# Performance work log

Hardware: AMD Instinct MI355X
Metric: run time of the kernel (lower is better)

Reference implementation:

```python
import jax, jax.numpy as jnp
import numpy as np

S, D, H1, H2, H3 = 4, 384, 160, 128, 96  # species, aev_length, hidden dims
B, A = 2048, 64  # conformations, atoms
CELU_ALPHA = 0.1


def setup_inputs() -> dict:
    key = jax.random.key(0)
    ks = jax.random.split(key, 10)
    scale = 0.1
    return {
        "species": jax.random.randint(ks[0], (B, A), 0, S),
        "aev": jax.random.normal(ks[1], (B, A, D), dtype=jnp.float32),
        "W1": jax.random.normal(ks[2], (S, D, H1), dtype=jnp.float32) * scale,
        "b1": jax.random.normal(ks[3], (S, H1), dtype=jnp.float32) * scale,
        "W2": jax.random.normal(ks[4], (S, H1, H2), dtype=jnp.float32) * scale,
        "b2": jax.random.normal(ks[5], (S, H2), dtype=jnp.float32) * scale,
        "W3": jax.random.normal(ks[6], (S, H2, H3), dtype=jnp.float32) * scale,
        "b3": jax.random.normal(ks[7], (S, H3), dtype=jnp.float32) * scale,
        "W4": jax.random.normal(ks[8], (S, H3, 1), dtype=jnp.float32) * scale,
        "b4": jax.random.normal(ks[9], (S, 1), dtype=jnp.float32) * scale,
    }


def _celu(x):
    return jax.nn.celu(x, alpha=CELU_ALPHA)


def reference(species, aev, W1, b1, W2, b2, W3, b3, W4, b4):
    # species: [B, A] int; aev: [B, A, D]
    b, a, d = aev.shape
    x = aev.reshape(b * a, d)  # flatten(0, 1)
    # Run every species-expert MLP on all atoms (dense, jit-friendly), then
    # gather the row matching each atom's species. Same math as the masked
    # index_select/scatter loop in the original (padding_fill=0, reducer=sum).
    h = _celu(jnp.einsum('nd,sdh->snh', x, W1) + b1[:, None, :])   # [S, N, H1]
    h = _celu(jnp.einsum('snh,sho->sno', h, W2) + b2[:, None, :])  # [S, N, H2]
    h = _celu(jnp.einsum('snh,sho->sno', h, W3) + b3[:, None, :])  # [S, N, H3]
    y = (jnp.einsum('snh,sho->sno', h, W4) + b4[:, None, :])[..., 0]  # [S, N]
    sp_flat = species.reshape(1, b * a)
    per_atom = jnp.take_along_axis(y, sp_flat, axis=0)[0]  # [N]
    per_atom = per_atom.reshape(b, a)
    energies = per_atom.sum(axis=1)  # reducer=torch.sum over dim=1
    return species, energies
```

## Files before the change

kernel.cpp:

```cpp
#include <hip/hip_runtime.h>
#include <hip/hip_bf16.h>


#define NSP   4
#define DIM   384
#define NH1   160
#define NH2   128
#define NH3   96
#define DIMP  392
#define NH1P  168
#define NH2P  136
#define NH3P  104
#define NATOM (2048 * 64)
#define NCONF 2048

typedef __attribute__((ext_vector_type(8))) short short8;
typedef __attribute__((ext_vector_type(4))) float f32x4;

__device__ __forceinline__ unsigned short f2bf(float f) {
  union { float f; unsigned u; } v; v.f = f;
  unsigned r = v.u + 0x7fffu + ((v.u >> 16) & 1u);
  return (unsigned short)(r >> 16);
}
__device__ __forceinline__ float bf2f(unsigned short h) {
  union { unsigned u; float f; } v; v.u = ((unsigned)h) << 16;
  return v.f;
}


__global__ void k_count(const int* __restrict__ sp, int* __restrict__ hdr,
                        float* __restrict__ out_species) {
  const int i = blockIdx.x * 256 + threadIdx.x;
  const int s = sp[i];
  out_species[i] = (float)s;
  __shared__ int cnt[NSP];
  if (threadIdx.x < NSP) cnt[threadIdx.x] = 0;
  __syncthreads();
  const int lane = threadIdx.x & 63;
#pragma unroll
  for (int sv = 0; sv < NSP; ++sv) {
    unsigned long long m = __ballot(s == sv);
    if (lane == 0) atomicAdd(&cnt[sv], __popcll(m));
  }
  __syncthreads();
  if (threadIdx.x < NSP) atomicAdd(&hdr[threadIdx.x], cnt[threadIdx.x]);
}

__global__ void k_scan(int* hdr) {
  if (threadIdx.x == 0 && blockIdx.x == 0) {
    int ro = 0, po = 0;
    for (int s = 0; s < NSP; ++s) {
      hdr[4 + s]  = ro;
      hdr[9 + s]  = po;
      hdr[14 + s] = ro;
      int cs = hdr[s];
      ro += cs;
      po += (cs + 63) & ~63;
    }
    hdr[8]  = ro;
    hdr[13] = po;
  }
}

__global__ void k_scatter(const int* __restrict__ sp, int* __restrict__ hdr,
                          int* __restrict__ sorted) {
  const int i = blockIdx.x * 256 + threadIdx.x;
  const int s = sp[i];
  const int lane = threadIdx.x & 63, wave = threadIdx.x >> 6;
  __shared__ int wcnt[4][NSP];
  __shared__ int wbase[4][NSP];
  const unsigned long long below = (1ull << lane) - 1ull;
  int myrank = 0;
#pragma unroll
  for (int sv = 0; sv < NSP; ++sv) {
    unsigned long long m = __ballot(s == sv);
    if (sv == s) myrank = __popcll(m & below);
    if (lane == 0) wcnt[wave][sv] = __popcll(m);
  }
  __syncthreads();
  if (threadIdx.x < NSP) {
    const int sv = threadIdx.x;
    const int tot = wcnt[0][sv] + wcnt[1][sv] + wcnt[2][sv] + wcnt[3][sv];
    int off = atomicAdd(&hdr[14 + sv], tot);
#pragma unroll
    for (int w = 0; w < 4; ++w) { wbase[w][sv] = off; off += wcnt[w][sv]; }
  }
  __syncthreads();
  sorted[wbase[wave][s] + myrank] = i;
}

__global__ void k_wcvt(const float* __restrict__ src, unsigned short* __restrict__ dst,
                       int K, int N, int total) {
  int i = blockIdx.x * 256 + threadIdx.x;
  if (i < total) {
    int kn = K * N;
    int s = i / kn, r = i - s * kn;
    int n = r / K, k = r - n * K;
    dst[i] = f2bf(src[s * kn + k * N + n]);
  }
}


template <int K, int KP, int NOUT, int NOUTP, bool DOCELU>
__device__ __forceinline__ void layer(const unsigned short* __restrict__ sIn,
                                      const unsigned short* __restrict__ Wt,
                                      const float* __restrict__ bias,
                                      unsigned short* __restrict__ sOut,
                                      int wave, int lane) {
  constexpr int NF = NOUT / 16;
  constexpr int NOWN = (NF + 3) / 4;
  const int c = lane & 15, q = lane >> 4;
  const int kb = q * 8;

  f32x4 acc[4][NOWN];
#pragma unroll
  for (int m = 0; m < 4; ++m)
#pragma unroll
    for (int i = 0; i < NOWN; ++i) acc[m][i] = (f32x4){0.f, 0.f, 0.f, 0.f};

  for (int k0 = 0; k0 < K; k0 += 32) {
    short8 a[4];
#pragma unroll
    for (int m = 0; m < 4; ++m)
      a[m] = *(const short8*)(sIn + (m * 16 + c) * KP + k0 + kb);
#pragma unroll
    for (int i = 0; i < NOWN; ++i) {
      int f = wave + 4 * i;
      if (f < NF) {
        short8 b = *(const short8*)(Wt + (f * 16 + c) * K + k0 + kb);
#pragma unroll
        for (int m = 0; m < 4; ++m)
          acc[m][i] = __builtin_amdgcn_mfma_f32_16x16x32_bf16(a[m], b, acc[m][i], 0, 0, 0);
      }
    }
  }

#pragma unroll
  for (int i = 0; i < NOWN; ++i) {
    int f = wave + 4 * i;
    if (f < NF) {
      int col = f * 16 + c;
      float bv = bias[col];
#pragma unroll
      for (int m = 0; m < 4; ++m) {
#pragma unroll
        for (int j = 0; j < 4; ++j) {
          float v = acc[m][i][j] + bv;
          if (DOCELU) v = v > 0.f ? v : 0.1f * (__expf(10.f * v) - 1.f);
          sOut[(m * 16 + q * 4 + j) * NOUTP + col] = f2bf(v);
        }
      }
    }
  }
}

#define LDSA (64 * DIMP * 2)
#define LDSH (64 * NH1P * 2)

__global__ __launch_bounds__(256) void k_mlp(
    const int* __restrict__ hdr, const int* __restrict__ sorted,
    const float* __restrict__ aev,
    const unsigned short* __restrict__ Wt1, const unsigned short* __restrict__ Wt2,
    const unsigned short* __restrict__ Wt3,
    const float* __restrict__ b1, const float* __restrict__ b2,
    const float* __restrict__ b3,
    const float* __restrict__ W4, const float* __restrict__ b4,
    float* __restrict__ energy) {
  __shared__ __align__(16) unsigned char smem[LDSA + LDSH];
  unsigned short* sA = (unsigned short*)smem;
  unsigned short* sH = (unsigned short*)(smem + LDSA);

  const int tid = threadIdx.x, wave = tid >> 6, lane = tid & 63;
  const int t64 = blockIdx.x << 6;
  if (t64 >= hdr[13]) return;
  const int s = (t64 >= hdr[10]) + (t64 >= hdr[11]) + (t64 >= hdr[12]);
  const int seg0 = t64 - hdr[9 + s];
  const int base = hdr[4 + s] + seg0;
  const int cnt = hdr[s];

  for (int rr = 0; rr < 16; ++rr) {
    const int row = (wave << 4) + rr;
    const bool valid = (seg0 + row) < cnt;
    const int atom = valid ? sorted[base + row] : 0;
    const float4* src = (const float4*)(aev + (size_t)atom * DIM);
#pragma unroll
    for (int jj = 0; jj < 2; ++jj) {
      const int idx = lane + (jj << 6);
      if (idx < 96) {
        float4 v = valid ? src[idx] : make_float4(0.f, 0.f, 0.f, 0.f);
        uint2 w;
        w.x = (unsigned)f2bf(v.x) | ((unsigned)f2bf(v.y) << 16);
        w.y = (unsigned)f2bf(v.z) | ((unsigned)f2bf(v.w) << 16);
        *(uint2*)(sA + row * DIMP + idx * 4) = w;
      }
    }
  }
  __syncthreads();

  layer<DIM, DIMP, NH1, NH1P, true>(sA, Wt1 + s * NH1 * DIM, b1 + s * NH1, sH, wave, lane);
  __syncthreads();
  layer<NH1, NH1P, NH2, NH2P, true>(sH, Wt2 + s * NH2 * NH1, b2 + s * NH2, sA, wave, lane);
  __syncthreads();
  layer<NH2, NH2P, NH3, NH3P, true>(sA, Wt3 + s * NH3 * NH2, b3 + s * NH3, sH, wave, lane);
  __syncthreads();

  {
    const int row = tid >> 2, part = tid & 3;
    if (seg0 + row < cnt) {
      const float* w4 = W4 + s * NH3 + part * 24;
      const unsigned short* hrow = sH + row * NH3P + part * 24;
      float acc = 0.f;
#pragma unroll
      for (int u = 0; u < 3; ++u) {
        short8 h = *(const short8*)(hrow + u * 8);
#pragma unroll
        for (int e = 0; e < 8; ++e)
          acc += bf2f((unsigned short)h[e]) * w4[u * 8 + e];
      }
      acc += __shfl_xor(acc, 1);
      acc += __shfl_xor(acc, 2);
      if (part == 0) {
        const int atom = sorted[base + row];
        atomicAdd(&energy[atom >> 6], acc + b4[s]);
      }
    }
  }
}


extern "C" void kernel_launch(void* const* d_in, const int* in_sizes, int n_in,
                              void* d_out, int out_size, void* d_ws, size_t ws_size,
                              hipStream_t stream) {
  const int* species = (const int*)d_in[0];
  const float* aev = (const float*)d_in[1];
  const float* W1 = (const float*)d_in[2];
  const float* b1 = (const float*)d_in[3];
  const float* W2 = (const float*)d_in[4];
  const float* b2 = (const float*)d_in[5];
  const float* W3 = (const float*)d_in[6];
  const float* b3 = (const float*)d_in[7];
  const float* W4 = (const float*)d_in[8];
  const float* b4 = (const float*)d_in[9];

  int* hdr = (int*)d_ws;
  int* sorted = (int*)((char*)d_ws + 128);
  unsigned short* Wt1 = (unsigned short*)((char*)d_ws + 128 + (size_t)NATOM * 4);
  unsigned short* Wt2 = Wt1 + NSP * NH1 * DIM;
  unsigned short* Wt3 = Wt2 + NSP * NH2 * NH1;

  float* out_species = (float*)d_out;
  float* energy = (float*)d_out + NATOM;

  hipMemsetAsync(d_ws, 0, 128, stream);
  hipMemsetAsync(energy, 0, NCONF * sizeof(float), stream);

  k_count<<<NATOM / 256, 256, 0, stream>>>(species, hdr, out_species);
  k_scan<<<1, 64, 0, stream>>>(hdr);
  k_scatter<<<NATOM / 256, 256, 0, stream>>>(species, hdr, sorted);
  k_wcvt<<<(NSP * NH1 * DIM + 255) / 256, 256, 0, stream>>>(W1, Wt1, DIM, NH1, NSP * NH1 * DIM);
  k_wcvt<<<(NSP * NH2 * NH1 + 255) / 256, 256, 0, stream>>>(W2, Wt2, NH1, NH2, NSP * NH2 * NH1);
  k_wcvt<<<(NSP * NH3 * NH2 + 255) / 256, 256, 0, stream>>>(W3, Wt3, NH2, NH3, NSP * NH3 * NH2);

  k_mlp<<<2052, 256, 0, stream>>>(hdr, sorted, aev, Wt1, Wt2, Wt3,
                                  b1, b2, b3, W4, b4, energy);
}
```

Before: 504.0 us.

## Give each wave its own 16-row tile, read AEV directly into MFMA operands

```diff
diff --git a/kernel.cpp b/kernel.cpp
--- a/kernel.cpp
+++ b/kernel.cpp
@@ -7,13 +7,17 @@
 #define NH1   160
 #define NH2   128
 #define NH3   96
-#define DIMP  392
 #define NH1P  168
 #define NH2P  136
 #define NH3P  104
 #define NATOM (2048 * 64)
 #define NCONF 2048
 
+#define XBYTES (16 * NH1P * 2)
+#define YBYTES (16 * NH2P * 2)
+#define WAVE_LDS (XBYTES + YBYTES)
+#define BLOCK_LDS (4 * WAVE_LDS)
+
 typedef __attribute__((ext_vector_type(8))) short short8;
 typedef __attribute__((ext_vector_type(4))) float f32x4;
 
@@ -25,6 +29,17 @@
 __device__ __forceinline__ float bf2f(unsigned short h) {
   union { unsigned u; float f; } v; v.u = ((unsigned)h) << 16;
   return v.f;
+}
+__device__ __forceinline__ short8 cvt8(float4 x, float4 y) {
+  union { short8 v; __hip_bfloat162 h[4]; } u;
+  u.h[0] = __float22bfloat162_rn(make_float2(x.x, x.y));
+  u.h[1] = __float22bfloat162_rn(make_float2(x.z, x.w));
+  u.h[2] = __float22bfloat162_rn(make_float2(y.x, y.y));
+  u.h[3] = __float22bfloat162_rn(make_float2(y.z, y.w));
+  return u.v;
+}
+__device__ __forceinline__ float celu01(float v) {
+  return v > 0.f ? v : 0.1f * (__expf(10.f * v) - 1.f);
 }
 
 
@@ -89,75 +104,60 @@
   sorted[wbase[wave][s] + myrank] = i;
 }
 
-__global__ void k_wcvt(const float* __restrict__ src, unsigned short* __restrict__ dst,
-                       int K, int N, int total) {
+#define N1TOT (NSP * NH1 * DIM)
+#define N2TOT (NSP * NH2 * NH1)
+#define N3TOT (NSP * NH3 * NH2)
+#define NWTOT (N1TOT + N2TOT + N3TOT)
+
+__device__ __forceinline__ void wcvt1(const float* src, unsigned short* dst,
+                                      int i, int K, int N) {
+  int kn = K * N;
+  int s = i / kn, r = i - s * kn;
+  int n = r / K, k = r - n * K;
+  dst[i] = f2bf(src[s * kn + k * N + n]);
+}
+
+__global__ void k_wcvt_all(const float* __restrict__ W1, const float* __restrict__ W2,
+                           const float* __restrict__ W3,
+                           unsigned short* __restrict__ Wt1, unsigned short* __restrict__ Wt2,
+                           unsigned short* __restrict__ Wt3) {
   int i = blockIdx.x * 256 + threadIdx.x;
-  if (i < total) {
-    int kn = K * N;
-    int s = i / kn, r = i - s * kn;
-    int n = r / K, k = r - n * K;
-    dst[i] = f2bf(src[s * kn + k * N + n]);
-  }
-}
-
-
-template <int K, int KP, int NOUT, int NOUTP, bool DOCELU>
-__device__ __forceinline__ void layer(const unsigned short* __restrict__ sIn,
-                                      const unsigned short* __restrict__ Wt,
-                                      const float* __restrict__ bias,
-                                      unsigned short* __restrict__ sOut,
-                                      int wave, int lane) {
+  if (i < N1TOT) wcvt1(W1, Wt1, i, DIM, NH1);
+  else if (i < N1TOT + N2TOT) wcvt1(W2, Wt2, i - N1TOT, NH1, NH2);
+  else if (i < NWTOT) wcvt1(W3, Wt3, i - N1TOT - N2TOT, NH2, NH3);
+}
+
+
+template <int K, int KP, int NOUT, int NOUTP>
+__device__ __forceinline__ void layerL(const unsigned short* __restrict__ sIn,
+                                       const unsigned short* __restrict__ Wt,
+                                       const float* __restrict__ bias,
+                                       unsigned short* __restrict__ sOut,
+                                       int c, int q) {
   constexpr int NF = NOUT / 16;
-  constexpr int NOWN = (NF + 3) / 4;
-  const int c = lane & 15, q = lane >> 4;
-  const int kb = q * 8;
-
-  f32x4 acc[4][NOWN];
-#pragma unroll
-  for (int m = 0; m < 4; ++m)
-#pragma unroll
-    for (int i = 0; i < NOWN; ++i) acc[m][i] = (f32x4){0.f, 0.f, 0.f, 0.f};
-
+  f32x4 acc[NF];
+#pragma unroll
+  for (int f = 0; f < NF; ++f) acc[f] = (f32x4){0.f, 0.f, 0.f, 0.f};
+
+#pragma unroll 2
   for (int k0 = 0; k0 < K; k0 += 32) {
-    short8 a[4];
-#pragma unroll
-    for (int m = 0; m < 4; ++m)
-      a[m] = *(const short8*)(sIn + (m * 16 + c) * KP + k0 + kb);
-#pragma unroll
-    for (int i = 0; i < NOWN; ++i) {
-      int f = wave + 4 * i;
-      if (f < NF) {
-        short8 b = *(const short8*)(Wt + (f * 16 + c) * K + k0 + kb);
-#pragma unroll
-        for (int m = 0; m < 4; ++m)
-          acc[m][i] = __builtin_amdgcn_mfma_f32_16x16x32_bf16(a[m], b, acc[m][i], 0, 0, 0);
-      }
-    }
-  }
-
-#pragma unroll
-  for (int i = 0; i < NOWN; ++i) {
-    int f = wave + 4 * i;
-    if (f < NF) {
-      int col = f * 16 + c;
-      float bv = bias[col];
-#pragma unroll
-      for (int m = 0; m < 4; ++m) {
-#pragma unroll
-        for (int j = 0; j < 4; ++j) {
-          float v = acc[m][i][j] + bv;
-          if (DOCELU) v = v > 0.f ? v : 0.1f * (__expf(10.f * v) - 1.f);
-          sOut[(m * 16 + q * 4 + j) * NOUTP + col] = f2bf(v);
-        }
-      }
-    }
-  }
-}
-
-#define LDSA (64 * DIMP * 2)
-#define LDSH (64 * NH1P * 2)
-
-__global__ __launch_bounds__(256) void k_mlp(
+    short8 a = *(const short8*)(sIn + c * KP + k0 + q * 8);
+#pragma unroll
+    for (int f = 0; f < NF; ++f) {
+      short8 b = *(const short8*)(Wt + (f * 16 + c) * K + k0 + q * 8);
+      acc[f] = __builtin_amdgcn_mfma_f32_16x16x32_bf16(a, b, acc[f], 0, 0, 0);
+    }
+  }
+#pragma unroll
+  for (int f = 0; f < NF; ++f) {
+    float bv = bias[f * 16 + c];
+#pragma unroll
+    for (int j = 0; j < 4; ++j)
+      sOut[(4 * q + j) * NOUTP + f * 16 + c] = f2bf(celu01(acc[f][j] + bv));
+  }
+}
+
+__global__ __launch_bounds__(256, 4) void k_mlp(
     const int* __restrict__ hdr, const int* __restrict__ sorted,
     const float* __restrict__ aev,
     const unsigned short* __restrict__ Wt1, const unsigned short* __restrict__ Wt2,
@@ -166,64 +166,66 @@
     const float* __restrict__ b3,
     const float* __restrict__ W4, const float* __restrict__ b4,
     float* __restrict__ energy) {
-  __shared__ __align__(16) unsigned char smem[LDSA + LDSH];
-  unsigned short* sA = (unsigned short*)smem;
-  unsigned short* sH = (unsigned short*)(smem + LDSA);
-
+  __shared__ __align__(16) unsigned char smem[BLOCK_LDS];
   const int tid = threadIdx.x, wave = tid >> 6, lane = tid & 63;
+  const int c = lane & 15, q = lane >> 4;
+  unsigned short* hX = (unsigned short*)(smem + wave * WAVE_LDS);
+  unsigned short* hY = (unsigned short*)(smem + wave * WAVE_LDS + XBYTES);
+
   const int t64 = blockIdx.x << 6;
   if (t64 >= hdr[13]) return;
   const int s = (t64 >= hdr[10]) + (t64 >= hdr[11]) + (t64 >= hdr[12]);
-  const int seg0 = t64 - hdr[9 + s];
-  const int base = hdr[4 + s] + seg0;
-  const int cnt = hdr[s];
-
-  for (int rr = 0; rr < 16; ++rr) {
-    const int row = (wave << 4) + rr;
-    const bool valid = (seg0 + row) < cnt;
-    const int atom = valid ? sorted[base + row] : 0;
-    const float4* src = (const float4*)(aev + (size_t)atom * DIM);
-#pragma unroll
-    for (int jj = 0; jj < 2; ++jj) {
-      const int idx = lane + (jj << 6);
-      if (idx < 96) {
-        float4 v = valid ? src[idx] : make_float4(0.f, 0.f, 0.f, 0.f);
-        uint2 w;
-        w.x = (unsigned)f2bf(v.x) | ((unsigned)f2bf(v.y) << 16);
-        w.y = (unsigned)f2bf(v.z) | ((unsigned)f2bf(v.w) << 16);
-        *(uint2*)(sA + row * DIMP + idx * 4) = w;
+  const int seg0 = t64 - hdr[9 + s] + wave * 16;
+  const int cnt  = hdr[s];
+  const bool valid = (seg0 + c) < cnt;
+  const int sidx = valid ? (hdr[4 + s] + seg0 + c) : hdr[4 + s];
+  const int atom = sorted[sidx];
+  const float* __restrict__ arow = aev + (size_t)atom * DIM;
+
+  {
+    const unsigned short* __restrict__ Wt = Wt1 + s * NH1 * DIM;
+    f32x4 acc[10];
+#pragma unroll
+    for (int f = 0; f < 10; ++f) acc[f] = (f32x4){0.f, 0.f, 0.f, 0.f};
+#pragma unroll 2
+    for (int k0 = 0; k0 < DIM; k0 += 32) {
+      float4 fa = *(const float4*)(arow + k0 + q * 8);
+      float4 fb = *(const float4*)(arow + k0 + q * 8 + 4);
+      short8 a = cvt8(fa, fb);
+#pragma unroll
+      for (int f = 0; f < 10; ++f) {
+        short8 b = *(const short8*)(Wt + (f * 16 + c) * DIM + k0 + q * 8);
+        acc[f] = __builtin_amdgcn_mfma_f32_16x16x32_bf16(a, b, acc[f], 0, 0, 0);
       }
     }
-  }
-  __syncthreads();
-
-  layer<DIM, DIMP, NH1, NH1P, true>(sA, Wt1 + s * NH1 * DIM, b1 + s * NH1, sH, wave, lane);
-  __syncthreads();
-  layer<NH1, NH1P, NH2, NH2P, true>(sH, Wt2 + s * NH2 * NH1, b2 + s * NH2, sA, wave, lane);
-  __syncthreads();
-  layer<NH2, NH2P, NH3, NH3P, true>(sA, Wt3 + s * NH3 * NH2, b3 + s * NH3, sH, wave, lane);
-  __syncthreads();
+    const float* bias = b1 + s * NH1;
+#pragma unroll
+    for (int f = 0; f < 10; ++f) {
+      float bv = bias[f * 16 + c];
+#pragma unroll
+      for (int j = 0; j < 4; ++j)
+        hX[(4 * q + j) * NH1P + f * 16 + c] = f2bf(celu01(acc[f][j] + bv));
+    }
+  }
+
+  layerL<NH1, NH1P, NH2, NH2P>(hX, Wt2 + s * NH2 * NH1, b2 + s * NH2, hY, c, q);
+  layerL<NH2, NH2P, NH3, NH3P>(hY, Wt3 + s * NH3 * NH2, b3 + s * NH3, hX, c, q);
 
   {
-    const int row = tid >> 2, part = tid & 3;
-    if (seg0 + row < cnt) {
-      const float* w4 = W4 + s * NH3 + part * 24;
-      const unsigned short* hrow = sH + row * NH3P + part * 24;
-      float acc = 0.f;
-#pragma unroll
-      for (int u = 0; u < 3; ++u) {
-        short8 h = *(const short8*)(hrow + u * 8);
-#pragma unroll
-        for (int e = 0; e < 8; ++e)
-          acc += bf2f((unsigned short)h[e]) * w4[u * 8 + e];
-      }
-      acc += __shfl_xor(acc, 1);
-      acc += __shfl_xor(acc, 2);
-      if (part == 0) {
-        const int atom = sorted[base + row];
-        atomicAdd(&energy[atom >> 6], acc + b4[s]);
-      }
-    }
+    const float* __restrict__ w4 = W4 + s * NH3 + q * 24;
+    const unsigned short* __restrict__ hrow = hX + c * NH3P + q * 24;
+    float dot = 0.f;
+#pragma unroll
+    for (int u = 0; u < 3; ++u) {
+      short8 h = *(const short8*)(hrow + u * 8);
+#pragma unroll
+      for (int e = 0; e < 8; ++e)
+        dot += bf2f((unsigned short)h[e]) * w4[u * 8 + e];
+    }
+    dot += __shfl_xor(dot, 16);
+    dot += __shfl_xor(dot, 32);
+    if (q == 0 && valid)
+      atomicAdd(&energy[atom >> 6], dot + b4[s]);
   }
 }
 
@@ -245,8 +247,8 @@
   int* hdr = (int*)d_ws;
   int* sorted = (int*)((char*)d_ws + 128);
   unsigned short* Wt1 = (unsigned short*)((char*)d_ws + 128 + (size_t)NATOM * 4);
-  unsigned short* Wt2 = Wt1 + NSP * NH1 * DIM;
-  unsigned short* Wt3 = Wt2 + NSP * NH2 * NH1;
+  unsigned short* Wt2 = Wt1 + N1TOT;
+  unsigned short* Wt3 = Wt2 + N2TOT;
 
   float* out_species = (float*)d_out;
   float* energy = (float*)d_out + NATOM;
@@ -257,9 +259,7 @@
   k_count<<<NATOM / 256, 256, 0, stream>>>(species, hdr, out_species);
   k_scan<<<1, 64, 0, stream>>>(hdr);
   k_scatter<<<NATOM / 256, 256, 0, stream>>>(species, hdr, sorted);
-  k_wcvt<<<(NSP * NH1 * DIM + 255) / 256, 256, 0, stream>>>(W1, Wt1, DIM, NH1, NSP * NH1 * DIM);
-  k_wcvt<<<(NSP * NH2 * NH1 + 255) / 256, 256, 0, stream>>>(W2, Wt2, NH1, NH2, NSP * NH2 * NH1);
-  k_wcvt<<<(NSP * NH3 * NH2 + 255) / 256, 256, 0, stream>>>(W3, Wt3, NH2, NH3, NSP * NH3 * NH2);
+  k_wcvt_all<<<(NWTOT + 255) / 256, 256, 0, stream>>>(W1, W2, W3, Wt1, Wt2, Wt3);
 
   k_mlp<<<2052, 256, 0, stream>>>(hdr, sorted, aev, Wt1, Wt2, Wt3,
                                   b1, b2, b3, W4, b4, energy);
```

Result: faster. 461.9 us (-8.3%).
